# Kernel tuning notes

Hardware: AMD Instinct MI355X
Metric: run time of the kernel (lower is better)

## Reference

```python
import jax, jax.numpy as jnp
import numpy as np

B, T = 64, 1000
RNN_DIM, EMB_DIM, ATT_DIM, LOC_DIM, KSIZE = 1024, 512, 128, 32, 31


def setup_inputs() -> dict:
    key = jax.random.key(0)
    ks = jax.random.split(key, 8)
    s = 0.02  # small init scale for weights
    return {
        "attention_hidden_state": jax.random.normal(ks[0], (B, RNN_DIM), jnp.float32),
        "memory": jax.random.normal(ks[1], (B, T, EMB_DIM), jnp.float32),
        "processed_memory": jax.random.normal(ks[2], (B, T, ATT_DIM), jnp.float32),
        "attention_weights_cat": jax.random.uniform(ks[3], (B, 2, T), jnp.float32),
        "mask": jnp.zeros((B, T), dtype=bool),
        "W_query": jax.random.normal(ks[4], (ATT_DIM, RNN_DIM), jnp.float32) * s,
        "conv_w": jax.random.normal(ks[5], (LOC_DIM, 2, KSIZE), jnp.float32) * s,
        "W_loc": jax.random.normal(ks[6], (ATT_DIM, LOC_DIM), jnp.float32) * s,
        "v": jax.random.normal(ks[7], (1, ATT_DIM), jnp.float32) * s,
    }


def reference(attention_hidden_state, memory, processed_memory,
              attention_weights_cat, mask, W_query, conv_w, W_loc, v):
    # processed_query: (B, 1, ATT_DIM)
    pq = (attention_hidden_state @ W_query.T)[:, None, :]
    # location features: conv1d over (B, 2, T), SAME padding, no bias
    loc = jax.lax.conv_general_dilated(
        attention_weights_cat, conv_w,
        window_strides=(1,), padding="SAME",
        dimension_numbers=("NCH", "OIH", "NCH"))  # (B, LOC_DIM, T)
    loc = jnp.einsum("bct,ac->bta", loc, W_loc)  # (B, T, ATT_DIM)
    # energies: v . tanh(pq + loc + processed_memory) -> (B, T)
    energy = jnp.einsum("bta,oa->bt", jnp.tanh(pq + loc + processed_memory), v)
    energy = jnp.where(mask, -jnp.inf, energy)
    attention_weights = jax.nn.softmax(energy, axis=1)  # (B, T)
    attention_context = jnp.einsum("bt,bte->be", attention_weights, memory)
    return attention_context, attention_weights
```

## Files before the change

### kernel.cpp

```cpp
#include <hip/hip_runtime.h>
#include <hip/hip_bf16.h>
#include <math.h>

#define B 64
#define T 1000
#define RNN_DIM 1024
#define EMB_DIM 512
#define ATT_DIM 128
#define LOC_DIM 32
#define KSIZE 31
#define PAD 15
#define ET 64
#define ESL 32

__global__ __launch_bounds__(256) void pq_kernel(
    const float* __restrict__ hidden,
    const float* __restrict__ Wq,
    float* __restrict__ pq)
{
    int gwave = (blockIdx.x * blockDim.x + threadIdx.x) >> 6;
    int lane  = threadIdx.x & 63;
    int b = gwave >> 7;
    int a = gwave & 127;

    const float4* h4 = (const float4*)(hidden + (size_t)b * RNN_DIM);
    const float4* w4 = (const float4*)(Wq + (size_t)a * RNN_DIM);

    float acc = 0.f;
#pragma unroll
    for (int j = 0; j < 4; ++j) {
        float4 h = h4[j * 64 + lane];
        float4 w = w4[j * 64 + lane];
        acc += h.x * w.x + h.y * w.y + h.z * w.z + h.w * w.w;
    }
#pragma unroll
    for (int off = 32; off > 0; off >>= 1)
        acc += __shfl_down(acc, off, 64);
    if (lane == 0) pq[gwave] = acc;
}

__global__ __launch_bounds__(256) void energy_kernel(
    const float* __restrict__ aw,
    const float* __restrict__ cw,
    const float* __restrict__ wl,
    const float* __restrict__ pq,
    const float* __restrict__ pm,
    const float* __restrict__ v,
    float* __restrict__ energy)
{
    __shared__ float aw_lds[2][ET + 2 * PAD];
    __shared__ float cw_lds[LOC_DIM][2][KSIZE];
    __shared__ float wl_lds[ATT_DIM][36];
    __shared__ float pq_lds[ATT_DIM];
    __shared__ float v_lds[ATT_DIM];
    __shared__ float loc_lds[ET][36];

    const int b   = blockIdx.x;
    const int t0  = blockIdx.y * ET;
    const int tid = threadIdx.x;

    const int TL = tid >> 4;
    const int AL = tid & 15;
    const int tb = TL * 4;

    float acc_e[4][8];
#pragma unroll
    for (int jj = 0; jj < 4; ++jj) {
        const int t = t0 + tb + jj;
        const bool ok = (t < T);
        const float* prow = pm + ((size_t)b * T + (ok ? t : 0)) * ATT_DIM + AL;
#pragma unroll
        for (int aa = 0; aa < 8; ++aa)
            acc_e[jj][aa] = ok ? prow[16 * aa] : 0.f;
    }

    for (int i = tid; i < LOC_DIM * 2 * KSIZE; i += 256)
        ((float*)cw_lds)[i] = cw[i];
    for (int i = tid; i < ATT_DIM * LOC_DIM; i += 256)
        wl_lds[i >> 5][i & 31] = wl[i];
    if (tid < ATT_DIM) {
        pq_lds[tid] = pq[b * ATT_DIM + tid];
        v_lds[tid]  = v[tid];
    }
    for (int i = tid; i < 2 * (ET + 2 * PAD); i += 256) {
        int ch = i / (ET + 2 * PAD);
        int p  = i % (ET + 2 * PAD);
        int t  = t0 + p - PAD;
        aw_lds[ch][p] = (t >= 0 && t < T) ? aw[(size_t)b * 2 * T + ch * T + t] : 0.f;
    }
    __syncthreads();

    {
        const int c  = tid & 31;
        const int tg = tid >> 5;
        float acc[8];
#pragma unroll
        for (int j = 0; j < 8; ++j) acc[j] = 0.f;
#pragma unroll
        for (int ch = 0; ch < 2; ++ch) {
            float awr[KSIZE + 7];
#pragma unroll
            for (int j = 0; j < KSIZE + 7; ++j) awr[j] = aw_lds[ch][tg * 8 + j];
#pragma unroll
            for (int k = 0; k < KSIZE; ++k) {
                float cv = cw_lds[c][ch][k];
#pragma unroll
                for (int j = 0; j < 8; ++j) acc[j] += cv * awr[k + j];
            }
        }
#pragma unroll
        for (int j = 0; j < 8; ++j) loc_lds[tg * 8 + j][c] = acc[j];
    }
    __syncthreads();

#pragma unroll
    for (int h = 0; h < 4; ++h) {
        float lrh[4][8];
#pragma unroll
        for (int jj = 0; jj < 4; ++jj) {
            *((float4*)&lrh[jj][0]) = *((const float4*)&loc_lds[tb + jj][8 * h]);
            *((float4*)&lrh[jj][4]) = *((const float4*)&loc_lds[tb + jj][8 * h + 4]);
        }
#pragma unroll
        for (int aa = 0; aa < 8; ++aa) {
            const int a = AL + 16 * aa;
            float4 w0 = *((const float4*)&wl_lds[a][8 * h]);
            float4 w1 = *((const float4*)&wl_lds[a][8 * h + 4]);
#pragma unroll
            for (int jj = 0; jj < 4; ++jj) {
                acc_e[jj][aa] +=
                      w0.x * lrh[jj][0] + w0.y * lrh[jj][1]
                    + w0.z * lrh[jj][2] + w0.w * lrh[jj][3]
                    + w1.x * lrh[jj][4] + w1.y * lrh[jj][5]
                    + w1.z * lrh[jj][6] + w1.w * lrh[jj][7];
            }
        }
    }

    float acc[4] = {0.f, 0.f, 0.f, 0.f};
#pragma unroll
    for (int aa = 0; aa < 8; ++aa) {
        const int a = AL + 16 * aa;
        const float pqa = pq_lds[a];
        const float va  = v_lds[a];
#pragma unroll
        for (int jj = 0; jj < 4; ++jj) {
            float e = acc_e[jj][aa] + pqa;
            float ex = __expf(2.f * e);
            float th = 1.f - 2.f * __builtin_amdgcn_rcpf(1.f + ex);
            acc[jj] += va * th;
        }
    }
#pragma unroll
    for (int jj = 0; jj < 4; ++jj) {
        float s = acc[jj];
        s += __shfl_xor(s, 1, 64);
        s += __shfl_xor(s, 2, 64);
        s += __shfl_xor(s, 4, 64);
        s += __shfl_xor(s, 8, 64);
        if (AL == 0) {
            int t = t0 + tb + jj;
            if (t < T) energy[b * T + t] = s;
        }
    }
}

__global__ __launch_bounds__(256) void softmax_kernel(
    const float* __restrict__ energy,
    const unsigned char* __restrict__ mask,
    float* __restrict__ out)
{
    int b   = blockIdx.x;
    int tid = threadIdx.x;

    __shared__ float red[4];
    float e[4];
    float mx = -INFINITY;
#pragma unroll
    for (int j = 0; j < 4; ++j) {
        int t = tid + j * 256;
        if (t < T) {
            float val = energy[b * T + t];
            if (mask[b * T + t]) val = -INFINITY;
            e[j] = val;
            mx = fmaxf(mx, val);
        } else e[j] = -INFINITY;
    }
#pragma unroll
    for (int off = 32; off > 0; off >>= 1)
        mx = fmaxf(mx, __shfl_down(mx, off, 64));
    if ((tid & 63) == 0) red[tid >> 6] = mx;
    __syncthreads();
    mx = fmaxf(fmaxf(red[0], red[1]), fmaxf(red[2], red[3]));
    __syncthreads();

    float sum = 0.f;
    float ex[4];
#pragma unroll
    for (int j = 0; j < 4; ++j) {
        ex[j] = (e[j] == -INFINITY) ? 0.f : expf(e[j] - mx);
        sum += ex[j];
    }
#pragma unroll
    for (int off = 32; off > 0; off >>= 1)
        sum += __shfl_down(sum, off, 64);
    if ((tid & 63) == 0) red[tid >> 6] = sum;
    __syncthreads();
    sum = red[0] + red[1] + red[2] + red[3];
    float inv = 1.f / sum;
#pragma unroll
    for (int j = 0; j < 4; ++j) {
        int t = tid + j * 256;
        if (t < T) out[B * EMB_DIM + b * T + t] = ex[j] * inv;
    }
}

__global__ __launch_bounds__(256) void context_kernel(
    const float* __restrict__ memory,
    const float* __restrict__ w,
    float* __restrict__ ctx)
{
    __shared__ float w_lds[1024];
    __shared__ float red[4][ESL];

    const int b   = blockIdx.x;
    const int e0  = blockIdx.y * ESL;
    const int tid = threadIdx.x;
    const int col = tid & 7;
    const int rg  = tid >> 3;

    for (int i = tid; i < 1024; i += 256)
        w_lds[i] = (i < T) ? w[b * T + i] : 0.f;
    __syncthreads();

    const float4* mem4 = (const float4*)(memory + (size_t)b * T * EMB_DIM + e0);

    float4 acc = {0.f, 0.f, 0.f, 0.f};
    float4 mbuf[8];
#pragma unroll 1
    for (int blk = 0; blk < 4; ++blk) {
        const int rbase = blk * 256 + rg;
#pragma unroll
        for (int u = 0; u < 8; ++u) {
            int r  = rbase + 32 * u;
            int rc = (r < T) ? r : (T - 1);
            mbuf[u] = mem4[(size_t)rc * 128 + col];
        }
#pragma unroll
        for (int u = 0; u < 8; ++u) {
            float wt = w_lds[rbase + 32 * u];
            acc.x += wt * mbuf[u].x; acc.y += wt * mbuf[u].y;
            acc.z += wt * mbuf[u].z; acc.w += wt * mbuf[u].w;
        }
    }

    acc.x += __shfl_xor(acc.x, 8, 64);  acc.x += __shfl_xor(acc.x, 16, 64);  acc.x += __shfl_xor(acc.x, 32, 64);
    acc.y += __shfl_xor(acc.y, 8, 64);  acc.y += __shfl_xor(acc.y, 16, 64);  acc.y += __shfl_xor(acc.y, 32, 64);
    acc.z += __shfl_xor(acc.z, 8, 64);  acc.z += __shfl_xor(acc.z, 16, 64);  acc.z += __shfl_xor(acc.z, 32, 64);
    acc.w += __shfl_xor(acc.w, 8, 64);  acc.w += __shfl_xor(acc.w, 16, 64);  acc.w += __shfl_xor(acc.w, 32, 64);

    if ((tid & 63) < 8)
        *((float4*)&red[tid >> 6][4 * col]) = acc;
    __syncthreads();
    if (tid < ESL) {
        float s = red[0][tid] + red[1][tid] + red[2][tid] + red[3][tid];
        ctx[b * EMB_DIM + e0 + tid] = s;
    }
}

extern "C" void kernel_launch(void* const* d_in, const int* in_sizes, int n_in,
                              void* d_out, int out_size, void* d_ws, size_t ws_size,
                              hipStream_t stream) {
    const float* hidden = (const float*)d_in[0];
    const float* memory = (const float*)d_in[1];
    const float* pm     = (const float*)d_in[2];
    const float* aw     = (const float*)d_in[3];
    const unsigned char* mask = (const unsigned char*)d_in[4];
    const float* Wq     = (const float*)d_in[5];
    const float* cw     = (const float*)d_in[6];
    const float* wl     = (const float*)d_in[7];
    const float* v      = (const float*)d_in[8];

    float* out = (float*)d_out;

    float* pq_ws     = (float*)d_ws;
    float* energy_ws = pq_ws + B * ATT_DIM;

    pq_kernel<<<dim3((B * ATT_DIM) / 4), dim3(256), 0, stream>>>(hidden, Wq, pq_ws);

    energy_kernel<<<dim3(B, (T + ET - 1) / ET), dim3(256), 0, stream>>>(
        aw, cw, wl, pq_ws, pm, v, energy_ws);

    softmax_kernel<<<dim3(B), dim3(256), 0, stream>>>(energy_ws, mask, out);

    context_kernel<<<dim3(B, EMB_DIM / ESL), dim3(256), 0, stream>>>(
        memory, out + B * EMB_DIM, out);
}
```

Before: 273.1 us.

## Fuse softmax into context kernel and double-buffer memory loads

Merges the softmax and context kernels into one launch. Each of the 16 column blocks per batch recomputes the softmax over energies, writes the weights to LDS, and only blockIdx.y==0 stores them to the output. The first tile of memory is loaded before the softmax reductions so its latency overlaps them, and the context loop becomes a ping-pong double-buffered sequence. It also switches to the fast __expf. This removes a launch and the round trip of the weights through global memory, at the cost of redundant softmax work and more registers.

```diff
diff --git a/kernel.cpp b/kernel.cpp
--- a/kernel.cpp
+++ b/kernel.cpp
@@ -165,63 +165,15 @@
     }
 }
 
-__global__ __launch_bounds__(256) void softmax_kernel(
+__global__ __launch_bounds__(256) void softmax_context_kernel(
+    const float* __restrict__ memory,
     const float* __restrict__ energy,
     const unsigned char* __restrict__ mask,
     float* __restrict__ out)
 {
-    int b   = blockIdx.x;
-    int tid = threadIdx.x;
-
-    __shared__ float red[4];
-    float e[4];
-    float mx = -INFINITY;
-#pragma unroll
-    for (int j = 0; j < 4; ++j) {
-        int t = tid + j * 256;
-        if (t < T) {
-            float val = energy[b * T + t];
-            if (mask[b * T + t]) val = -INFINITY;
-            e[j] = val;
-            mx = fmaxf(mx, val);
-        } else e[j] = -INFINITY;
-    }
-#pragma unroll
-    for (int off = 32; off > 0; off >>= 1)
-        mx = fmaxf(mx, __shfl_down(mx, off, 64));
-    if ((tid & 63) == 0) red[tid >> 6] = mx;
-    __syncthreads();
-    mx = fmaxf(fmaxf(red[0], red[1]), fmaxf(red[2], red[3]));
-    __syncthreads();
-
-    float sum = 0.f;
-    float ex[4];
-#pragma unroll
-    for (int j = 0; j < 4; ++j) {
-        ex[j] = (e[j] == -INFINITY) ? 0.f : expf(e[j] - mx);
-        sum += ex[j];
-    }
-#pragma unroll
-    for (int off = 32; off > 0; off >>= 1)
-        sum += __shfl_down(sum, off, 64);
-    if ((tid & 63) == 0) red[tid >> 6] = sum;
-    __syncthreads();
-    sum = red[0] + red[1] + red[2] + red[3];
-    float inv = 1.f / sum;
-#pragma unroll
-    for (int j = 0; j < 4; ++j) {
-        int t = tid + j * 256;
-        if (t < T) out[B * EMB_DIM + b * T + t] = ex[j] * inv;
-    }
-}
-
-__global__ __launch_bounds__(256) void context_kernel(
-    const float* __restrict__ memory,
-    const float* __restrict__ w,
-    float* __restrict__ ctx)
-{
     __shared__ float w_lds[1024];
-    __shared__ float red[4][ESL];
+    __shared__ float sred[4];
+    __shared__ float cred[4][ESL];
 
     const int b   = blockIdx.x;
     const int e0  = blockIdx.y * ESL;
@@ -229,30 +181,90 @@
     const int col = tid & 7;
     const int rg  = tid >> 3;
 
-    for (int i = tid; i < 1024; i += 256)
-        w_lds[i] = (i < T) ? w[b * T + i] : 0.f;
-    __syncthreads();
+    float e[4];
+#pragma unroll
+    for (int j = 0; j < 4; ++j) {
+        int t = tid + j * 256;
+        bool ok = (t < T);
+        float val = ok ? energy[b * T + t] : -INFINITY;
+        unsigned char m = ok ? mask[b * T + t] : (unsigned char)1;
+        e[j] = (ok && !m) ? val : -INFINITY;
+    }
 
     const float4* mem4 = (const float4*)(memory + (size_t)b * T * EMB_DIM + e0);
+    float4 mA[8], mB[8];
+#pragma unroll
+    for (int u = 0; u < 8; ++u)
+        mA[u] = mem4[(size_t)(rg + 32 * u) * 128 + col];
+
+    float mx = fmaxf(fmaxf(e[0], e[1]), fmaxf(e[2], e[3]));
+#pragma unroll
+    for (int off = 32; off > 0; off >>= 1)
+        mx = fmaxf(mx, __shfl_down(mx, off, 64));
+    if ((tid & 63) == 0) sred[tid >> 6] = mx;
+    __syncthreads();
+    mx = fmaxf(fmaxf(sred[0], sred[1]), fmaxf(sred[2], sred[3]));
+    __syncthreads();
+
+    float sum = 0.f;
+    float ex[4];
+#pragma unroll
+    for (int j = 0; j < 4; ++j) {
+        ex[j] = (e[j] == -INFINITY) ? 0.f : __expf(e[j] - mx);
+        sum += ex[j];
+    }
+#pragma unroll
+    for (int off = 32; off > 0; off >>= 1)
+        sum += __shfl_down(sum, off, 64);
+    if ((tid & 63) == 0) sred[tid >> 6] = sum;
+    __syncthreads();
+    sum = sred[0] + sred[1] + sred[2] + sred[3];
+    float inv = 1.f / sum;
+
+#pragma unroll
+    for (int j = 0; j < 4; ++j) {
+        int t = tid + j * 256;
+        float wv = ex[j] * inv;
+        w_lds[t] = (t < T) ? wv : 0.f;
+        if (blockIdx.y == 0 && t < T)
+            out[B * EMB_DIM + b * T + t] = wv;
+    }
+    __syncthreads();
 
     float4 acc = {0.f, 0.f, 0.f, 0.f};
-    float4 mbuf[8];
-#pragma unroll 1
-    for (int blk = 0; blk < 4; ++blk) {
-        const int rbase = blk * 256 + rg;
-#pragma unroll
-        for (int u = 0; u < 8; ++u) {
-            int r  = rbase + 32 * u;
-            int rc = (r < T) ? r : (T - 1);
-            mbuf[u] = mem4[(size_t)rc * 128 + col];
-        }
-#pragma unroll
-        for (int u = 0; u < 8; ++u) {
-            float wt = w_lds[rbase + 32 * u];
-            acc.x += wt * mbuf[u].x; acc.y += wt * mbuf[u].y;
-            acc.z += wt * mbuf[u].z; acc.w += wt * mbuf[u].w;
-        }
-    }
+
+#define CTX_ISSUE(buf, base)                                              \
+    _Pragma("unroll")                                                     \
+    for (int u = 0; u < 8; ++u)                                           \
+        buf[u] = mem4[(size_t)((base) + rg + 32 * u) * 128 + col];
+
+#define CTX_ISSUE_CLAMP(buf, base)                                        \
+    _Pragma("unroll")                                                     \
+    for (int u = 0; u < 8; ++u) {                                         \
+        int r  = (base) + rg + 32 * u;                                    \
+        int rc = (r < T) ? r : (T - 1);                                   \
+        buf[u] = mem4[(size_t)rc * 128 + col];                            \
+    }
+
+#define CTX_CONSUME(buf, base)                                            \
+    _Pragma("unroll")                                                     \
+    for (int u = 0; u < 8; ++u) {                                         \
+        float wt = w_lds[(base) + rg + 32 * u];                           \
+        acc.x += wt * buf[u].x; acc.y += wt * buf[u].y;                   \
+        acc.z += wt * buf[u].z; acc.w += wt * buf[u].w;                   \
+    }
+
+    CTX_ISSUE(mB, 256)
+    CTX_CONSUME(mA, 0)
+    CTX_ISSUE(mA, 512)
+    CTX_CONSUME(mB, 256)
+    CTX_ISSUE_CLAMP(mB, 768)
+    CTX_CONSUME(mA, 512)
+    CTX_CONSUME(mB, 768)
+
+#undef CTX_ISSUE
+#undef CTX_ISSUE_CLAMP
+#undef CTX_CONSUME
 
     acc.x += __shfl_xor(acc.x, 8, 64);  acc.x += __shfl_xor(acc.x, 16, 64);  acc.x += __shfl_xor(acc.x, 32, 64);
     acc.y += __shfl_xor(acc.y, 8, 64);  acc.y += __shfl_xor(acc.y, 16, 64);  acc.y += __shfl_xor(acc.y, 32, 64);
@@ -260,11 +272,11 @@
     acc.w += __shfl_xor(acc.w, 8, 64);  acc.w += __shfl_xor(acc.w, 16, 64);  acc.w += __shfl_xor(acc.w, 32, 64);
 
     if ((tid & 63) < 8)
-        *((float4*)&red[tid >> 6][4 * col]) = acc;
+        *((float4*)&cred[tid >> 6][4 * col]) = acc;
     __syncthreads();
     if (tid < ESL) {
-        float s = red[0][tid] + red[1][tid] + red[2][tid] + red[3][tid];
-        ctx[b * EMB_DIM + e0 + tid] = s;
+        float s = cred[0][tid] + cred[1][tid] + cred[2][tid] + cred[3][tid];
+        out[b * EMB_DIM + e0 + tid] = s;
     }
 }
 
@@ -291,8 +303,6 @@
     energy_kernel<<<dim3(B, (T + ET - 1) / ET), dim3(256), 0, stream>>>(
         aw, cw, wl, pq_ws, pm, v, energy_ws);
 
-    softmax_kernel<<<dim3(B), dim3(256), 0, stream>>>(energy_ws, mask, out);
-
-    context_kernel<<<dim3(B, EMB_DIM / ESL), dim3(256), 0, stream>>>(
-        memory, out + B * EMB_DIM, out);
+    softmax_context_kernel<<<dim3(B, EMB_DIM / ESL), dim3(256), 0, stream>>>(
+        memory, energy_ws, mask, out);
 }
```

After: 267.8 us. Within noise of the previous version (-1.9%).
